# Kernel tuning notes

Hardware: AMD Instinct MI355X
Metric: run time of the kernel (lower is better)

Reference implementation:

```python
import jax, jax.numpy as jnp
import numpy as np

# Model constants (from source: model_dim=1024, head_dim=128, num_heads=8)
L = 8          # num layers (reduced from 16 for tractable reference memory)
T = 2048       # packed tokens, B == 1 (varlen)
DIM = 1024
NH = 8
NKV = 4        # GQA kv heads
HD = 128
KVD = NKV * HD
BLOCK = 128
WS = 3
WIN = WS * BLOCK           # sliding-window size for 'S' layers
ATTN_SCALE = 0.12
PATTERN = 'SSSL'
GATE_CH = 32
EPS = 1.1920929e-07        # torch F.rms_norm default eps = finfo(fp32).eps


def rms_norm(x):
    return x * jax.lax.rsqrt(jnp.mean(x * x, axis=-1, keepdims=True) + EPS)


def apply_rotary(x, cos, sin):
    # x: [T, H, HD]; cos/sin: [T, 1, HD//2]
    d = x.shape[-1] // 2
    x1, x2 = x[..., :d], x[..., d:]
    return jnp.concatenate([x1 * cos + x2 * sin, -x1 * sin + x2 * cos], axis=-1)


def has_ve(layer_idx, n_layer):
    return layer_idx % 2 == (n_layer - 1) % 2


def setup_inputs() -> dict:
    key = jax.random.key(0)
    ks = jax.random.split(key, 9)
    x = jax.random.normal(ks[0], (1, T, DIM), jnp.float32)
    ve = jax.random.normal(ks[1], (L, T, KVD), jnp.float32)
    s = DIM ** -0.5
    Wq = jax.random.normal(ks[2], (L, DIM, NH * HD), jnp.float32) * s
    Wk = jax.random.normal(ks[3], (L, DIM, KVD), jnp.float32) * s
    Wv = jax.random.normal(ks[4], (L, DIM, KVD), jnp.float32) * s
    Wo = jax.random.normal(ks[5], (L, NH * HD, DIM), jnp.float32) * (NH * HD) ** -0.5
    Wgate = jax.random.normal(ks[6], (L, GATE_CH, NKV), jnp.float32) * GATE_CH ** -0.5
    Wfc = jax.random.normal(ks[7], (L, DIM, 4 * DIM), jnp.float32) * s
    Wproj = jax.random.normal(ks[8], (L, 4 * DIM, DIM), jnp.float32) * (4 * DIM) ** -0.5
    # RoPE tables (absolute positions of the packed batch, as in the source)
    inv_freq = 1.0 / (10000.0 ** (jnp.arange(HD // 2, dtype=jnp.float32) / (HD // 2)))
    ang = jnp.arange(T, dtype=jnp.float32)[:, None] * inv_freq[None, :]
    cos = jnp.cos(ang)[:, None, :]
    sin = jnp.sin(ang)[:, None, :]
    # cu_seqlens: 4 packed documents of 512 tokens
    seqlens = jnp.array([0, 512, 1024, 1536, 2048], dtype=jnp.int32)
    return dict(x=x, ve=ve, Wq=Wq, Wk=Wk, Wv=Wv, Wo=Wo, Wgate=Wgate,
                Wfc=Wfc, Wproj=Wproj, cos=cos, sin=sin, seqlens=seqlens)


def reference(x, ve, Wq, Wk, Wv, Wo, Wgate, Wfc, Wproj, cos, sin, seqlens):
    h = x[0]  # [T, DIM], B == 1 (varlen packing)
    pos = jnp.arange(T)
    doc = jnp.searchsorted(seqlens, pos, side='right') - 1
    diff = pos[:, None] - pos[None, :]
    base = (diff >= 0) & (doc[:, None] == doc[None, :])   # causal within doc
    mask_S = base & (diff <= WIN)                         # sliding window
    neg = jnp.float32(-1e30)
    rep = NH // NKV
    for l in range(L):
        xn = rms_norm(h)
        q = (xn @ Wq[l]).reshape(T, NH, HD)
        k = (xn @ Wk[l]).reshape(T, NKV, HD)
        v = (xn @ Wv[l]).reshape(T, NKV, HD)
        if has_ve(l, L):
            gate = 2.0 * jax.nn.sigmoid(xn[:, :GATE_CH] @ Wgate[l])  # [T, NKV]
            v = v + gate[:, :, None] * ve[l].reshape(T, NKV, HD)
        q = rms_norm(apply_rotary(q, cos, sin))
        k = rms_norm(apply_rotary(k, cos, sin))
        k = jnp.repeat(k, rep, axis=1)   # GQA -> full heads
        v2 = jnp.repeat(v, rep, axis=1)
        scores = jnp.einsum('thd,shd->hts', q, k) * ATTN_SCALE  # [NH, T, T]
        mask = mask_S if PATTERN[l % len(PATTERN)] == 'S' else base
        scores = jnp.where(mask[None], scores, neg)
        p = jax.nn.softmax(scores, axis=-1)
        y = jnp.einsum('hts,shd->thd', p, v2).reshape(T, NH * HD)
        h = h + y @ Wo[l]
        m = jnp.square(jax.nn.relu(rms_norm(h) @ Wfc[l]))  # relu(x)^2 MLP
        h = h + m @ Wproj[l]
    return h[None]
```

## Files before the change

### kernel.cpp

```cpp
#include <hip/hip_runtime.h>
#include <hip/hip_bf16.h>
#include <cstdint>
#include <cstddef>

#define TT     2048
#define DMODEL 1024
#define NHQ    8
#define HD     128
#define KVD    512
#define WIN    384
#define EPSF   1.1920929e-07f
#define SCALE  0.12f

typedef __attribute__((ext_vector_type(8))) short bf16x8;
typedef __attribute__((ext_vector_type(4))) float f32x4;

#define WAITV(N)  asm volatile("s_waitcnt vmcnt(" #N ")" ::: "memory")

__device__ __forceinline__ float b2f(unsigned short u) {
    unsigned int i = ((unsigned int)u) << 16; float f; __builtin_memcpy(&f, &i, 4); return f;
}
__device__ __forceinline__ unsigned short f2b(float f) {
    unsigned int i; __builtin_memcpy(&i, &f, 4);
    unsigned int r = (i + 0x7fffu + ((i >> 16) & 1u)) >> 16;
    return (unsigned short)r;
}

__device__ __forceinline__ void gl_lds16(const unsigned short* g, unsigned short* l) {
    __builtin_amdgcn_global_load_lds(
        (const __attribute__((address_space(1))) unsigned int*)g,
        (__attribute__((address_space(3))) unsigned int*)l, 16, 0, 0);
}
__device__ __forceinline__ void gl_lds16f(const float* g, float* l) {
    __builtin_amdgcn_global_load_lds(
        (const __attribute__((address_space(1))) unsigned int*)g,
        (__attribute__((address_space(3))) unsigned int*)l, 16, 0, 0);
}

__global__ __launch_bounds__(512)
void convT_k(const float* __restrict__ Wq, const float* __restrict__ Wk,
             const float* __restrict__ Wv, const float* __restrict__ Wo,
             const float* __restrict__ Wfc, const float* __restrict__ Wproj,
             unsigned short* __restrict__ Bqkv, unsigned short* __restrict__ Bo,
             unsigned short* __restrict__ Bfc, unsigned short* __restrict__ Bproj)
{
    __shared__ float lt[128 * 128];
    const int bid = blockIdx.x, tid = threadIdx.x, l = blockIdx.y;

    const float* W; unsigned short* Wt; int K, N, t, nbase;
    if (bid < 64)         { W = Wq    + (size_t)l * 1024 * 1024; Wt = Bqkv  + (size_t)l * 2048 * 1024; K = 1024; N = 1024; t = bid;       nbase = 0;    }
    else if (bid < 96)    { W = Wk    + (size_t)l * 1024 * 512;  Wt = Bqkv  + (size_t)l * 2048 * 1024; K = 1024; N = 512;  t = bid - 64;  nbase = 1024; }
    else if (bid < 128)   { W = Wv    + (size_t)l * 1024 * 512;  Wt = Bqkv  + (size_t)l * 2048 * 1024; K = 1024; N = 512;  t = bid - 96;  nbase = 1536; }
    else if (bid < 192)   { W = Wo    + (size_t)l * 1024 * 1024; Wt = Bo    + (size_t)l * 1024 * 1024; K = 1024; N = 1024; t = bid - 128; nbase = 0;    }
    else if (bid < 448)   { W = Wfc   + (size_t)l * 1024 * 4096; Wt = Bfc   + (size_t)l * 4096 * 1024; K = 1024; N = 4096; t = bid - 192; nbase = 0;    }
    else                  { W = Wproj + (size_t)l * 4096 * 1024; Wt = Bproj + (size_t)l * 1024 * 4096; K = 4096; N = 1024; t = bid - 448; nbase = 0;    }

    const int ktiles = K >> 7;
    const int kt0 = (t % ktiles) * 128, nt0 = (t / ktiles) * 128;

    const int lane = tid & 63, w = tid >> 6;
    const int lhi = lane >> 5;
    const int lc  = lane & 31;

    #pragma unroll
    for (int rd = 0; rd < 8; ++rd) {
        const int k = rd * 16 + w * 2 + lhi;
        const int csrc = lc ^ ((k >> 3) & 31);
        const float* src = W + (size_t)(kt0 + k) * N + nt0 + csrc * 4;
        float* dst = lt + (size_t)(rd * 16 + w * 2) * 128;
        gl_lds16f(src, dst);
    }
    __syncthreads();

    #pragma unroll
    for (int i = 0; i < 4; ++i) {
        int flat = i * 512 + tid;
        int n = flat >> 4, kc = (flat & 15) * 8;
        const int c = ((n >> 2) ^ (kc >> 3)) & 31;
        const float* rp = lt + (size_t)kc * 128 + c * 4 + (n & 3);
        unsigned short o[8];
        #pragma unroll
        for (int j = 0; j < 8; ++j) o[j] = f2b(rp[j * 128]);
        *(uint4*)(Wt + (size_t)(nbase + nt0 + n) * K + kt0 + kc) = *(const uint4*)o;
    }
}

template<int EPI>
__global__ __launch_bounds__(256, 2)
void gemm4(const unsigned short* __restrict__ A, const unsigned short* __restrict__ Bt,
           unsigned short* __restrict__ Cp, int K, int ksplit, int Ntot)
{
    __shared__ unsigned short As[2 * 128 * 64];
    __shared__ unsigned short Bs[2 * 128 * 64];
    const int BUF = 128 * 64;
    const int tid = threadIdx.x, lane = tid & 63, wv = tid >> 6;

    const int gx = gridDim.x;
    const int nwg = gx * gridDim.y;
    const int ihw = blockIdx.y * gx + blockIdx.x;
    const int q = nwg >> 3, r = nwg & 7;
    const int xcd = ihw & 7, pos = ihw >> 3;
    const int lg = (xcd < r) ? xcd * (q + 1) + pos
                             : r * (q + 1) + (xcd - r) * q + pos;
    const int m0 = (lg % gx) * 128, n0 = (lg / gx) * 128;

    const int kbeg = blockIdx.z * ksplit;
    const int NT = ksplit >> 6;

    const int wr = (wv >> 1) * 64, wc = (wv & 1) * 64;
    const int l15 = lane & 15, g = lane >> 4;
    const int srow = lane >> 3;
    const int sxor = (((lane & 7) ^ srow) << 3);

    const unsigned short* gA0 = A  + (size_t)(m0 + wv * 32 + srow) * K + sxor;
    const unsigned short* gB0 = Bt + (size_t)(n0 + wv * 32 + srow) * K + sxor;

    auto stage = [&](int t) {
        const int b = t & 1;
        const size_t k = (size_t)kbeg + ((size_t)t << 6);
        unsigned short* la = As + b * BUF + (wv * 32) * 64;
        unsigned short* lb = Bs + b * BUF + (wv * 32) * 64;
        #pragma unroll
        for (int c = 0; c < 4; ++c) {
            gl_lds16(gA0 + (size_t)(c * 8) * K + k, la + c * 8 * 64);
            gl_lds16(gB0 + (size_t)(c * 8) * K + k, lb + c * 8 * 64);
        }
    };

    f32x4 acc[4][4] = {};

    stage(0);
    for (int t = 0; t < NT; ++t) {
        if (t + 1 < NT) { stage(t + 1); WAITV(8); }
        else            { WAITV(0); }
        __builtin_amdgcn_s_barrier();

        const unsigned short* Ac = As + (t & 1) * BUF;
        const unsigned short* Bc = Bs + (t & 1) * BUF;
        bf16x8 af[4][2], bfv[4][2];
        #pragma unroll
        for (int mi = 0; mi < 4; ++mi) {
            const int row = wr + mi * 16 + l15, x = row & 7;
            #pragma unroll
            for (int kk = 0; kk < 2; ++kk)
                af[mi][kk] = *(const bf16x8*)(Ac + row * 64 + (((kk * 4 + g) ^ x) << 3));
        }
        #pragma unroll
        for (int ni = 0; ni < 4; ++ni) {
            const int row = wc + ni * 16 + l15, x = row & 7;
            #pragma unroll
            for (int kk = 0; kk < 2; ++kk)
                bfv[ni][kk] = *(const bf16x8*)(Bc + row * 64 + (((kk * 4 + g) ^ x) << 3));
        }
        __builtin_amdgcn_s_setprio(1);
        #pragma unroll
        for (int kk = 0; kk < 2; ++kk)
            #pragma unroll
            for (int mi = 0; mi < 4; ++mi)
                #pragma unroll
                for (int ni = 0; ni < 4; ++ni)
                    acc[mi][ni] = __builtin_amdgcn_mfma_f32_16x16x32_bf16(af[mi][kk], bfv[ni][kk], acc[mi][ni], 0, 0, 0);
        __builtin_amdgcn_s_setprio(0);
        __builtin_amdgcn_s_barrier();
    }

    unsigned short* Cz = Cp + (size_t)blockIdx.z * TT * Ntot;
    #pragma unroll
    for (int mi = 0; mi < 4; ++mi)
        #pragma unroll
        for (int ni = 0; ni < 4; ++ni)
            #pragma unroll
            for (int r2 = 0; r2 < 4; ++r2) {
                int row = m0 + wr + mi * 16 + g * 4 + r2;
                int col = n0 + wc + ni * 16 + l15;
                size_t idx = (size_t)row * Ntot + col;
                float v = acc[mi][ni][r2];
                if (EPI == 0) Cz[idx] = f2b(v);
                else {
                    float z = v > 0.f ? v * v : 0.f;
                    Cz[idx] = f2b(z);
                }
            }
}

__global__ __launch_bounds__(256)
void rmsnormF_k(float* __restrict__ h, const unsigned short* __restrict__ part, int nz,
                unsigned short* __restrict__ xn)
{
    const int t = blockIdx.x, tid = threadIdx.x;
    const size_t idx = (size_t)t * (DMODEL / 4) + tid;
    float4 v = ((const float4*)h)[idx];
    for (int z = 0; z < nz; ++z) {
        ushort4 p = ((const ushort4*)part)[idx + (size_t)z * (TT * DMODEL / 4)];
        v.x += b2f(p.x); v.y += b2f(p.y); v.z += b2f(p.z); v.w += b2f(p.w);
    }
    if (nz > 0) ((float4*)h)[idx] = v;

    float ss = v.x*v.x + v.y*v.y + v.z*v.z + v.w*v.w;
    #pragma unroll
    for (int m = 1; m < 64; m <<= 1) ss += __shfl_xor(ss, m);
    __shared__ float red[4];
    if ((tid & 63) == 0) red[tid >> 6] = ss;
    __syncthreads();
    float tot = red[0] + red[1] + red[2] + red[3];
    float rs = rsqrtf(tot * (1.f / DMODEL) + EPSF);
    unsigned short o[4] = { f2b(v.x*rs), f2b(v.y*rs), f2b(v.z*rs), f2b(v.w*rs) };
    *(ushort4*)(xn + (size_t)t * DMODEL + tid * 4) = *(const ushort4*)o;
}

__global__ __launch_bounds__(256)
void reduce_add_k(float* __restrict__ h, const unsigned short* __restrict__ part, int nz)
{
    const int i = blockIdx.x * 256 + threadIdx.x;
    float4 hv = ((float4*)h)[i];
    for (int z = 0; z < nz; ++z) {
        ushort4 p = ((const ushort4*)part)[i + (size_t)z * (TT * DMODEL / 4)];
        hv.x += b2f(p.x); hv.y += b2f(p.y); hv.z += b2f(p.z); hv.w += b2f(p.w);
    }
    ((float4*)h)[i] = hv;
}

__global__ __launch_bounds__(128)
void post_qkv_k(const unsigned short* __restrict__ qkv,
                const float* __restrict__ cosb, const float* __restrict__ sinb,
                unsigned short* __restrict__ qn, unsigned short* __restrict__ kn)
{
    const size_t S2 = (size_t)TT * 2048;
    const int t = blockIdx.x, tid = threadIdx.x;
    __shared__ float cs[64], sn[64];
    if (tid < 64) { cs[tid] = cosb[t * 64 + tid]; sn[tid] = sinb[t * 64 + tid]; }
    __syncthreads();
    if (tid < 96) {
        const int hid = tid >> 3, sub = tid & 7;
        const unsigned short* src; unsigned short* dst;
        if (hid < 8) { src = qkv + (size_t)t * 2048 + hid * 128;              dst = qn + (size_t)t * 1024 + hid * 128; }
        else         { src = qkv + (size_t)t * 2048 + 1024 + (hid - 8) * 128; dst = kn + (size_t)t * 512 + (hid - 8) * 128; }
        float o1[8], o2[8], ssum = 0.f;
        #pragma unroll
        for (int j = 0; j < 8; ++j) {
            int jj = sub * 8 + j;
            float x1 = b2f(src[jj])      + b2f(src[jj + S2]);
            float x2 = b2f(src[jj + 64]) + b2f(src[jj + 64 + S2]);
            float c = cs[jj], s = sn[jj];
            o1[j] = x1 * c + x2 * s;
            o2[j] = -x1 * s + x2 * c;
            ssum += o1[j]*o1[j] + o2[j]*o2[j];
        }
        ssum += __shfl_xor(ssum, 1); ssum += __shfl_xor(ssum, 2); ssum += __shfl_xor(ssum, 4);
        float rs = rsqrtf(ssum * (1.f / HD) + EPSF);
        #pragma unroll
        for (int j = 0; j < 8; ++j) {
            int jj = sub * 8 + j;
            dst[jj]      = f2b(o1[j] * rs);
            dst[jj + 64] = f2b(o2[j] * rs);
        }
    }
}

__global__ __launch_bounds__(256)
void vtrans2_k(const unsigned short* __restrict__ qkv, const unsigned short* __restrict__ xn,
               const float* __restrict__ Wgate, const float* __restrict__ vel, int hasve,
               unsigned short* __restrict__ vt)
{
    const size_t S2 = (size_t)TT * 2048;
    __shared__ unsigned short lt[64][72];
    __shared__ float gate_s[64];
    const int t0 = blockIdx.x * 64, c0 = blockIdx.y * 64, tid = threadIdx.x;
    const int gi = c0 >> 7;

    if (hasve && tid < 64) {
        const int t = t0 + tid;
        float a = 0.f;
        #pragma unroll
        for (int c = 0; c < 32; ++c) a += b2f(xn[(size_t)t * DMODEL + c]) * Wgate[c * 4 + gi];
        gate_s[tid] = 2.f / (1.f + __expf(-a));
    }
    __syncthreads();

    #pragma unroll
    for (int i = 0; i < 2; ++i) {
        int r = (tid >> 3) + i * 32;
        int c = (tid & 7) * 8;
        const int t = t0 + r, ch = c0 + c;
        size_t off = (size_t)t * 2048 + 1536 + ch;
        bf16x8 pa = *(const bf16x8*)(qkv + off);
        bf16x8 pb = *(const bf16x8*)(qkv + off + S2);
        float g = hasve ? gate_s[r] : 0.f;
        #pragma unroll
        for (int j = 0; j < 8; ++j) {
            float vv = b2f(((unsigned short*)&pa)[j]) + b2f(((unsigned short*)&pb)[j]);
            if (hasve) vv += g * vel[(size_t)t * KVD + ch + j];
            lt[c + j][r] = f2b(vv);
        }
    }
    __syncthreads();
    #pragma unroll
    for (int i = 0; i < 2; ++i) {
        int r = (tid >> 3) + i * 32;
        int c = (tid & 7) * 8;
        *(bf16x8*)(vt + (size_t)(c0 + r) * TT + t0 + c) = *(const bf16x8*)(&lt[r][c]);
    }
}

__global__ __launch_bounds__(256)
void attn_k(const unsigned short* __restrict__ qn, const unsigned short* __restrict__ kn,
            const unsigned short* __restrict__ vt, unsigned short* __restrict__ y,
            const int* __restrict__ seqlens, int isS)
{
    __shared__ float Ot[4][16][132];
    const int tid = threadIdx.x, w = tid >> 6, lane = tid & 63;
    const int h = blockIdx.y, hkv = h >> 1;
    const int qr = (blockIdx.x * 4 + w) * 16;
    const int s1 = seqlens[1], s2 = seqlens[2], s3 = seqlens[3];
    const int l15 = lane & 15, g = lane >> 4;

    bf16x8 qf[4];
    #pragma unroll
    for (int kk = 0; kk < 4; ++kk)
        qf[kk] = *(const bf16x8*)(qn + (size_t)(qr + l15) * 1024 + h * HD + kk * 32 + g * 8);

    const int row = qr + l15;
    const int drow = (row >= s1) + (row >= s2) + (row >= s3);

    int dq = (qr >= s1) + (qr >= s2) + (qr >= s3);
    int dstart = dq == 0 ? 0 : (dq == 1 ? s1 : (dq == 2 ? s2 : s3));
    int smin = dstart;
    if (isS) { int wlo = qr - WIN; if (wlo > smin) smin = wlo; }
    if (smin < 0) smin = 0;
    const int smax = qr + 16;

    f32x4 acc[8] = {};
    float mrow = -1e30f, lrow = 0.f;

    for (int s0 = smin & ~31; s0 < smax; s0 += 32) {
        f32x4 S[2] = {};
        __builtin_amdgcn_s_setprio(1);
        #pragma unroll
        for (int nb = 0; nb < 2; ++nb) {
            int srow = s0 + nb * 16 + l15;
            #pragma unroll
            for (int kk = 0; kk < 4; ++kk) {
                bf16x8 kf = *(const bf16x8*)(kn + (size_t)srow * KVD + hkv * HD + kk * 32 + g * 8);
                S[nb] = __builtin_amdgcn_mfma_f32_16x16x32_bf16(kf, qf[kk], S[nb], 0, 0, 0);
            }
        }
        __builtin_amdgcn_s_setprio(0);

        float sv[2][4];
        #pragma unroll
        for (int nb = 0; nb < 2; ++nb)
            #pragma unroll
            for (int r = 0; r < 4; ++r) {
                int s = s0 + nb * 16 + 4 * g + r;
                int dcol = (s >= s1) + (s >= s2) + (s >= s3);
                bool valid = (s <= row) && (dcol == drow) && (!isS || (row - s) <= WIN);
                sv[nb][r] = valid ? S[nb][r] * SCALE : -1e30f;
            }

        float pm = sv[0][0];
        #pragma unroll
        for (int r = 1; r < 4; ++r) pm = fmaxf(pm, sv[0][r]);
        #pragma unroll
        for (int r = 0; r < 4; ++r) pm = fmaxf(pm, sv[1][r]);
        pm = fmaxf(pm, __shfl_xor(pm, 16));
        pm = fmaxf(pm, __shfl_xor(pm, 32));
        float mnew = fmaxf(mrow, pm);
        float scl2 = __expf(mrow - mnew);
        float p0[4], p1[4], ps = 0.f;
        #pragma unroll
        for (int r = 0; r < 4; ++r) {
            p0[r] = __expf(sv[0][r] - mnew);
            p1[r] = __expf(sv[1][r] - mnew);
            ps += p0[r] + p1[r];
        }
        ps += __shfl_xor(ps, 16);
        ps += __shfl_xor(ps, 32);
        lrow = lrow * scl2 + ps;
        mrow = mnew;
        #pragma unroll
        for (int nb2 = 0; nb2 < 8; ++nb2) acc[nb2] *= scl2;

        unsigned short pt[8];
        const int base = l15 + ((g & 1) << 5);
        #pragma unroll
        for (int jh = 0; jh < 2; ++jh)
            #pragma unroll
            for (int r = 0; r < 4; ++r) {
                float ta = __shfl(p0[r], base + 16 * jh);
                float tb = __shfl(p1[r], base + 16 * jh);
                pt[jh * 4 + r] = f2b(g >= 2 ? tb : ta);
            }
        bf16x8 pf;
        #pragma unroll
        for (int j = 0; j < 8; ++j) ((unsigned short*)&pf)[j] = pt[j];

        __builtin_amdgcn_s_setprio(1);
        #pragma unroll
        for (int nb2 = 0; nb2 < 8; ++nb2) {
            bf16x8 vf = *(const bf16x8*)(vt + (size_t)(hkv * HD + nb2 * 16 + l15) * TT + s0 + g * 8);
            acc[nb2] = __builtin_amdgcn_mfma_f32_16x16x32_bf16(vf, pf, acc[nb2], 0, 0, 0);
        }
        __builtin_amdgcn_s_setprio(0);
    }

    const float inv = 1.f / lrow;
    #pragma unroll
    for (int nb2 = 0; nb2 < 8; ++nb2)
        #pragma unroll
        for (int r = 0; r < 4; ++r)
            Ot[w][l15][nb2 * 16 + 4 * g + r] = acc[nb2][r] * inv;
    __syncthreads();
    const int qo = lane >> 2, dblk = (lane & 3) * 32;
    #pragma unroll
    for (int i4 = 0; i4 < 4; ++i4) {
        unsigned short ob[8];
        #pragma unroll
        for (int j = 0; j < 8; ++j) ob[j] = f2b(Ot[w][qo][dblk + i4 * 8 + j]);
        *(uint4*)(y + (size_t)(qr + qo) * 1024 + h * HD + dblk + i4 * 8) = *(const uint4*)ob;
    }
}

extern "C" void kernel_launch(void* const* d_in, const int* in_sizes, int n_in,
                              void* d_out, int out_size, void* d_ws, size_t ws_size,
                              hipStream_t stream)
{
    const float* x       = (const float*)d_in[0];
    const float* ve      = (const float*)d_in[1];
    const float* Wq      = (const float*)d_in[2];
    const float* Wk      = (const float*)d_in[3];
    const float* Wv      = (const float*)d_in[4];
    const float* Wo      = (const float*)d_in[5];
    const float* Wgate   = (const float*)d_in[6];
    const float* Wfc     = (const float*)d_in[7];
    const float* Wproj   = (const float*)d_in[8];
    const float* cosb    = (const float*)d_in[9];
    const float* sinb    = (const float*)d_in[10];
    const int*   seqlens = (const int*)d_in[11];

    float* h = (float*)d_out;
    char* ws = (char*)d_ws;
    unsigned short* xn    = (unsigned short*)(ws);
    unsigned short* qn    = (unsigned short*)(ws + (4ull  << 20));
    unsigned short* kn    = (unsigned short*)(ws + (8ull  << 20));
    unsigned short* vt    = (unsigned short*)(ws + (12ull << 20));
    unsigned short* yb    = (unsigned short*)(ws + (14ull << 20));
    unsigned short* mb    = (unsigned short*)(ws + (18ull << 20));
    unsigned short* part  = (unsigned short*)(ws + (34ull << 20));
    unsigned short* Bqkv  = (unsigned short*)(ws + (50ull  << 20));
    unsigned short* Bo    = (unsigned short*)(ws + (82ull  << 20));
    unsigned short* Bfc   = (unsigned short*)(ws + (98ull  << 20));
    unsigned short* Bproj = (unsigned short*)(ws + (162ull << 20));

    hipMemcpyAsync(h, x, (size_t)TT * DMODEL * sizeof(float), hipMemcpyDeviceToDevice, stream);

    convT_k<<<dim3(704, 8), 512, 0, stream>>>(Wq, Wk, Wv, Wo, Wfc, Wproj,
                                              Bqkv, Bo, Bfc, Bproj);

    for (int l = 0; l < 8; ++l) {
        int hasve = (l % 2) == 1;
        int isS   = (l % 4) != 3;

        rmsnormF_k<<<TT, 256, 0, stream>>>(h, part, l == 0 ? 0 : 4, xn);

        gemm4<0><<<dim3(16, 16, 2), 256, 0, stream>>>(xn, Bqkv + (size_t)l * 2048 * 1024,
                                                      part, 1024, 512, 2048);

        post_qkv_k<<<TT, 128, 0, stream>>>(part, cosb, sinb, qn, kn);

        vtrans2_k<<<dim3(32, 8), 256, 0, stream>>>(part, xn,
            Wgate + (size_t)l * 128, ve + (size_t)l * TT * KVD, hasve, vt);

        attn_k<<<dim3(32, 8), 256, 0, stream>>>(qn, kn, vt, yb, seqlens, isS);

        gemm4<0><<<dim3(16, 8, 4), 256, 0, stream>>>(yb, Bo + (size_t)l * 1024 * 1024,
                                                     part, 1024, 256, 1024);

        rmsnormF_k<<<TT, 256, 0, stream>>>(h, part, 4, xn);

        gemm4<2><<<dim3(16, 32, 1), 256, 0, stream>>>(xn, Bfc + (size_t)l * 4096 * 1024,
                                                      mb, 1024, 1024, 4096);

        gemm4<0><<<dim3(16, 8, 4), 256, 0, stream>>>(mb, Bproj + (size_t)l * 1024 * 4096,
                                                     part, 4096, 1024, 1024);
    }

    reduce_add_k<<<2048, 256, 0, stream>>>(h, part, 4);
}
```

Before: 1.395 ms.

## Split attention KV range across two blocks and merge partial softmax results

The attention kernel now splits each query tile's key range into two halves handled by separate blocks (grid z=2). Each block writes unnormalized fp32 accumulators plus its row max and row sum to workspace. A new merge kernel combines the two halves with log-sum-exp weighting and writes the bf16 output. This doubles the number of attention blocks to improve GPU occupancy, since the original grid had only 256 blocks. The cost is an extra kernel launch and extra fp32 global traffic for the partial results; workspace offsets shift to make room for them.

```diff
diff --git a/kernel.cpp b/kernel.cpp
--- a/kernel.cpp
+++ b/kernel.cpp
@@ -304,20 +304,15 @@
 
 __global__ __launch_bounds__(256)
 void attn_k(const unsigned short* __restrict__ qn, const unsigned short* __restrict__ kn,
-            const unsigned short* __restrict__ vt, unsigned short* __restrict__ y,
+            const unsigned short* __restrict__ vt,
+            float* __restrict__ pacc, float* __restrict__ pml,
             const int* __restrict__ seqlens, int isS)
 {
-    __shared__ float Ot[4][16][132];
     const int tid = threadIdx.x, w = tid >> 6, lane = tid & 63;
-    const int h = blockIdx.y, hkv = h >> 1;
+    const int h = blockIdx.y, hkv = h >> 1, z = blockIdx.z;
     const int qr = (blockIdx.x * 4 + w) * 16;
     const int s1 = seqlens[1], s2 = seqlens[2], s3 = seqlens[3];
     const int l15 = lane & 15, g = lane >> 4;
-
-    bf16x8 qf[4];
-    #pragma unroll
-    for (int kk = 0; kk < 4; ++kk)
-        qf[kk] = *(const bf16x8*)(qn + (size_t)(qr + l15) * 1024 + h * HD + kk * 32 + g * 8);
 
     const int row = qr + l15;
     const int drow = (row >= s1) + (row >= s2) + (row >= s3);
@@ -329,10 +324,28 @@
     if (smin < 0) smin = 0;
     const int smax = qr + 16;
 
+    const int base0 = smin & ~31;
+    const int ntiles = (smax - base0 + 31) >> 5;
+    const int tp = (ntiles + 1) >> 1;
+    const int tbeg = z ? tp : 0, tend = z ? ntiles : tp;
+
+    const size_t rowi = ((size_t)z * NHQ + h) * TT + row;
+
+    if (tbeg >= tend) {
+        if (lane < 16) { pml[rowi * 2] = -1e30f; pml[rowi * 2 + 1] = 0.f; }
+        return;
+    }
+
+    bf16x8 qf[4];
+    #pragma unroll
+    for (int kk = 0; kk < 4; ++kk)
+        qf[kk] = *(const bf16x8*)(qn + (size_t)(qr + l15) * 1024 + h * HD + kk * 32 + g * 8);
+
     f32x4 acc[8] = {};
     float mrow = -1e30f, lrow = 0.f;
 
-    for (int s0 = smin & ~31; s0 < smax; s0 += 32) {
+    for (int tt = tbeg; tt < tend; ++tt) {
+        const int s0 = base0 + tt * 32;
         f32x4 S[2] = {};
         __builtin_amdgcn_s_setprio(1);
         #pragma unroll
@@ -365,12 +378,13 @@
         pm = fmaxf(pm, __shfl_xor(pm, 16));
         pm = fmaxf(pm, __shfl_xor(pm, 32));
         float mnew = fmaxf(mrow, pm);
+        const float vany = (mnew > -1e29f) ? 1.f : 0.f;
         float scl2 = __expf(mrow - mnew);
         float p0[4], p1[4], ps = 0.f;
         #pragma unroll
         for (int r = 0; r < 4; ++r) {
-            p0[r] = __expf(sv[0][r] - mnew);
-            p1[r] = __expf(sv[1][r] - mnew);
+            p0[r] = vany * __expf(sv[0][r] - mnew);
+            p1[r] = vany * __expf(sv[1][r] - mnew);
             ps += p0[r] + p1[r];
         }
         ps += __shfl_xor(ps, 16);
@@ -403,21 +417,38 @@
         __builtin_amdgcn_s_setprio(0);
     }
 
-    const float inv = 1.f / lrow;
+    float* pa = pacc + rowi * HD;
     #pragma unroll
     for (int nb2 = 0; nb2 < 8; ++nb2)
-        #pragma unroll
-        for (int r = 0; r < 4; ++r)
-            Ot[w][l15][nb2 * 16 + 4 * g + r] = acc[nb2][r] * inv;
-    __syncthreads();
-    const int qo = lane >> 2, dblk = (lane & 3) * 32;
-    #pragma unroll
-    for (int i4 = 0; i4 < 4; ++i4) {
-        unsigned short ob[8];
-        #pragma unroll
-        for (int j = 0; j < 8; ++j) ob[j] = f2b(Ot[w][qo][dblk + i4 * 8 + j]);
-        *(uint4*)(y + (size_t)(qr + qo) * 1024 + h * HD + dblk + i4 * 8) = *(const uint4*)ob;
-    }
+        *(float4*)(pa + nb2 * 16 + 4 * g) = *(float4*)&acc[nb2];
+    if (lane < 16) { pml[rowi * 2] = mrow; pml[rowi * 2 + 1] = lrow; }
+}
+
+__global__ __launch_bounds__(256)
+void attn_merge_k(const float* __restrict__ pacc, const float* __restrict__ pml,
+                  unsigned short* __restrict__ y)
+{
+    const int r = blockIdx.x, tid = threadIdx.x;
+    const int h = tid >> 5, dg = (tid & 31) * 4;
+    const size_t i1 = ((size_t)0 * NHQ + h) * TT + r;
+    const size_t i2 = ((size_t)1 * NHQ + h) * TT + r;
+    const float m1 = pml[i1 * 2], l1 = pml[i1 * 2 + 1];
+    const float m2 = pml[i2 * 2], l2 = pml[i2 * 2 + 1];
+    const float M = fmaxf(m1, m2);
+    const float w1 = (l1 > 0.f) ? __expf(m1 - M) : 0.f;
+    const float w2 = (l2 > 0.f) ? __expf(m2 - M) : 0.f;
+    const float inv = 1.f / (w1 * l1 + w2 * l2);
+
+    float4 a1 = {0.f, 0.f, 0.f, 0.f}, a2 = {0.f, 0.f, 0.f, 0.f};
+    if (l1 > 0.f) a1 = *(const float4*)(pacc + i1 * HD + dg);
+    if (l2 > 0.f) a2 = *(const float4*)(pacc + i2 * HD + dg);
+
+    unsigned short o[4];
+    o[0] = f2b((w1 * a1.x + w2 * a2.x) * inv);
+    o[1] = f2b((w1 * a1.y + w2 * a2.y) * inv);
+    o[2] = f2b((w1 * a1.z + w2 * a2.z) * inv);
+    o[3] = f2b((w1 * a1.w + w2 * a2.w) * inv);
+    *(ushort4*)(y + (size_t)r * 1024 + h * HD + dg) = *(const ushort4*)o;
 }
 
 extern "C" void kernel_launch(void* const* d_in, const int* in_sizes, int n_in,
@@ -446,10 +477,12 @@
     unsigned short* yb    = (unsigned short*)(ws + (14ull << 20));
     unsigned short* mb    = (unsigned short*)(ws + (18ull << 20));
     unsigned short* part  = (unsigned short*)(ws + (34ull << 20));
-    unsigned short* Bqkv  = (unsigned short*)(ws + (50ull  << 20));
-    unsigned short* Bo    = (unsigned short*)(ws + (82ull  << 20));
-    unsigned short* Bfc   = (unsigned short*)(ws + (98ull  << 20));
-    unsigned short* Bproj = (unsigned short*)(ws + (162ull << 20));
+    float*          pacc  = (float*)(ws + (50ull << 20));
+    float*          pml   = (float*)(ws + (66ull << 20));
+    unsigned short* Bqkv  = (unsigned short*)(ws + (68ull  << 20));
+    unsigned short* Bo    = (unsigned short*)(ws + (100ull << 20));
+    unsigned short* Bfc   = (unsigned short*)(ws + (116ull << 20));
+    unsigned short* Bproj = (unsigned short*)(ws + (180ull << 20));
 
     hipMemcpyAsync(h, x, (size_t)TT * DMODEL * sizeof(float), hipMemcpyDeviceToDevice, stream);
 
@@ -470,7 +503,8 @@
         vtrans2_k<<<dim3(32, 8), 256, 0, stream>>>(part, xn,
             Wgate + (size_t)l * 128, ve + (size_t)l * TT * KVD, hasve, vt);
 
-        attn_k<<<dim3(32, 8), 256, 0, stream>>>(qn, kn, vt, yb, seqlens, isS);
+        attn_k<<<dim3(32, 8, 2), 256, 0, stream>>>(qn, kn, vt, pacc, pml, seqlens, isS);
+        attn_merge_k<<<TT, 256, 0, stream>>>(pacc, pml, yb);
 
         gemm4<0><<<dim3(16, 8, 4), 256, 0, stream>>>(yb, Bo + (size_t)l * 1024 * 1024,
                                                      part, 1024, 256, 1024);
```

Result: faster. 1.269 ms, median of 2 (-9.0%).
